# Kernel optimization log

Hardware: AMD Instinct MI355X
Metric: run time of the kernel (lower is better)

## Reference

```python
import jax, jax.numpy as jnp
import numpy as np

B, T, D_IN, H, E = 256, 512, 256, 256, 96  # batch, enc seq, input_size, hidden_size, num_embeddings


def setup_inputs() -> dict:
    key = jax.random.key(0)
    ks = jax.random.split(key, 12)
    s = 0.05
    return {
        "prev_h": jax.random.normal(ks[0], (B, H), jnp.float32),
        "prev_c": jax.random.normal(ks[1], (B, H), jnp.float32),
        "batch_H": jax.random.normal(ks[2], (B, T, D_IN), jnp.float32),
        "char_onehots": jax.random.uniform(ks[3], (B, E), jnp.float32),
        "W_i2h": jax.random.normal(ks[4], (H, D_IN), jnp.float32) * s,
        "W_h2h": jax.random.normal(ks[5], (H, H), jnp.float32) * s,
        "b_h2h": jax.random.normal(ks[6], (H,), jnp.float32) * s,
        "W_score": jax.random.normal(ks[7], (1, H), jnp.float32) * s,
        "W_ih": jax.random.normal(ks[8], (4 * H, D_IN + E), jnp.float32) * s,
        "W_hh": jax.random.normal(ks[9], (4 * H, H), jnp.float32) * s,
        "b_ih": jax.random.normal(ks[10], (4 * H,), jnp.float32) * s,
        "b_hh": jax.random.normal(ks[11], (4 * H,), jnp.float32) * s,
    }


def reference(prev_h, prev_c, batch_H, char_onehots,
              W_i2h, W_h2h, b_h2h, W_score, W_ih, W_hh, b_ih, b_hh):
    # additive attention over encoder features
    proj = jnp.einsum('btd,hd->bth', batch_H, W_i2h)          # [B,T,H]
    hid = prev_h @ W_h2h.T + b_h2h                             # [B,H]
    e = jnp.einsum('bth,oh->bto', jnp.tanh(proj + hid[:, None, :]), W_score)  # [B,T,1]
    alpha = jax.nn.softmax(e, axis=1)                          # [B,T,1]
    context = jnp.einsum('bt,btd->bd', alpha[..., 0], batch_H) # [B,D_IN]
    x = jnp.concatenate([context, char_onehots], axis=1)       # [B,D_IN+E]
    # LSTM cell step (PyTorch gate order: i, f, g, o)
    gates = x @ W_ih.T + b_ih + prev_h @ W_hh.T + b_hh         # [B,4H]
    i, f, g, o = jnp.split(gates, 4, axis=1)
    c_new = jax.nn.sigmoid(f) * prev_c + jax.nn.sigmoid(i) * jnp.tanh(g)
    h_new = jax.nn.sigmoid(o) * jnp.tanh(c_new)
    return (h_new, c_new, jnp.swapaxes(alpha, 1, 2))           # alpha -> [B,1,T]
```

## Files before the change

### kernel.cpp

```cpp
#include <hip/hip_runtime.h>

typedef __attribute__((ext_vector_type(8))) short short8;
typedef __attribute__((ext_vector_type(4))) float f32x4;

#define KPAD 40

#define WS_HID 0u
#define WS_P   262144u
#define WS_Z   786432u
#define WS_CTX 802816u
#define WS_WBF 1064960u

__device__ __forceinline__ unsigned cvtpk(float lo, float hi) {
    unsigned r;
    asm("v_cvt_pk_bf16_f32 %0, %1, %2" : "=v"(r) : "v"(lo), "v"(hi));
    return r;
}
__device__ __forceinline__ int4 pack8(float4 x0, float4 x1) {
    int4 q;
    q.x = (int)cvtpk(x0.x, x0.y);
    q.y = (int)cvtpk(x0.z, x0.w);
    q.z = (int)cvtpk(x1.x, x1.y);
    q.w = (int)cvtpk(x1.z, x1.w);
    return q;
}
__device__ __forceinline__ float tanh_fast(float x) {
    float e2 = __expf(2.f * x);
    return 1.f - 2.f * __builtin_amdgcn_rcpf(e2 + 1.f);
}
__device__ __forceinline__ float sigmoid_fast(float x) {
    return __builtin_amdgcn_rcpf(1.f + __expf(-x));
}

__global__ __launch_bounds__(256) void k_prep(
    const float* __restrict__ prev_h, const float* __restrict__ W_i2h,
    const float* __restrict__ W_h2h, const float* __restrict__ b_h2h,
    float* __restrict__ hid, int4* __restrict__ Wbf)
{
    int bid = blockIdx.x, tid = threadIdx.x;
    if (bid < 256) {
        __shared__ float ph[256];
        ph[tid] = prev_h[bid * 256 + tid];
        __syncthreads();
        float acc = b_h2h[tid];
        const float4* w = (const float4*)(W_h2h + tid * 256);
        #pragma unroll 8
        for (int k4 = 0; k4 < 64; ++k4) {
            float4 ww = w[k4];
            acc += ww.x * ph[k4*4+0] + ww.y * ph[k4*4+1] + ww.z * ph[k4*4+2] + ww.w * ph[k4*4+3];
        }
        hid[bid * 256 + tid] = acc;
    } else {
        int u = (bid - 256) * 256 + tid;
        int w = (u >> 11) & 3, cf = (u >> 9) & 3, ks = (u >> 6) & 7;
        int n = w * 64 + cf * 16 + (u & 15);
        int k0 = ks * 32 + ((u >> 4) & 3) * 8;
        float4 x0 = *(const float4*)(W_i2h + n * 256 + k0);
        float4 x1 = *(const float4*)(W_i2h + n * 256 + k0 + 4);
        Wbf[u] = pack8(x0, x1);
    }
}

__global__ __launch_bounds__(256, 2) void k_e(
    const float* __restrict__ BH, const int4* __restrict__ Wbf,
    const float* __restrict__ hid, const float* __restrict__ Wsc,
    float* __restrict__ p_out, float* __restrict__ zbuf)
{
    __shared__ short Afrag[2][8192];
    __shared__ float eps[2][128];

    const int tid = threadIdx.x;
    const int lane = tid & 63;
    const int w = tid >> 6;
    const int l15 = lane & 15, lg = lane >> 4;
    const int b = blockIdx.x;

    short8 breg[4][8];
    #pragma unroll
    for (int cf = 0; cf < 4; cf++)
        #pragma unroll
        for (int ks = 0; ks < 8; ks++) {
            const int4* ap = Wbf + (((w * 4 + cf) * 8 + ks) * 64 + lane);
            asm volatile("global_load_dwordx4 %0, %1, off"
                         : "=v"(breg[cf][ks]) : "v"(ap));
        }

    float4 la0[4], la1[4];
    auto issueA = [&](int t) {
        const float* base = BH + ((size_t)b * 512 + t * 32) * 256;
        #pragma unroll
        for (int q = 0; q < 4; q++) {
            int u = q * 256 + tid;
            int row = ((u >> 9) << 4) | (u & 15);
            int kb = ((u >> 6) & 7) * 32 + ((u >> 4) & 3) * 8;
            const float* p4 = base + row * 256 + kb;
            la0[q] = *(const float4*)p4;
            la1[q] = *(const float4*)(p4 + 4);
        }
    };
    auto writeA = [&](int buf) {
        #pragma unroll
        for (int q = 0; q < 4; q++) {
            int u = q * 256 + tid;
            *(int4*)&Afrag[buf][u * 8] = pack8(la0[q], la1[q]);
        }
    };

    issueA(0);
    asm volatile("s_waitcnt vmcnt(0)" ::: "memory");
    #pragma unroll
    for (int cf = 0; cf < 4; cf++)
        asm volatile("" : "+v"(breg[cf][0]), "+v"(breg[cf][1]), "+v"(breg[cf][2]),
                          "+v"(breg[cf][3]), "+v"(breg[cf][4]), "+v"(breg[cf][5]),
                          "+v"(breg[cf][6]), "+v"(breg[cf][7]));
    writeA(0);
    __syncthreads();

    float wsv[4], hd4[4];
    #pragma unroll
    for (int cf = 0; cf < 4; cf++) {
        int col = w * 64 + cf * 16 + l15;
        wsv[cf] = Wsc[col];
        hd4[cf] = hid[b * 256 + col];
    }

    for (int t = 0; t < 16; ++t) {
        const int cur = t & 1;
        if (t < 15) issueA(t + 1);

        f32x4 acc[2][4];
        #pragma unroll
        for (int rf = 0; rf < 2; rf++)
            #pragma unroll
            for (int cf = 0; cf < 4; cf++) acc[rf][cf] = (f32x4){0.f, 0.f, 0.f, 0.f};

        #pragma unroll
        for (int ks = 0; ks < 8; ++ks) {
            short8 af[2];
            #pragma unroll
            for (int rf = 0; rf < 2; rf++)
                af[rf] = *(const short8*)&Afrag[cur][(((rf * 8 + ks) * 64) + lane) * 8];
            #pragma unroll
            for (int rf = 0; rf < 2; rf++)
                #pragma unroll
                for (int cf = 0; cf < 4; cf++)
                    acc[rf][cf] = __builtin_amdgcn_mfma_f32_16x16x32_bf16(
                        af[rf], breg[cf][ks], acc[rf][cf], 0, 0, 0);
        }

        float esum[2][4];
        #pragma unroll
        for (int rf = 0; rf < 2; rf++)
            #pragma unroll
            for (int r = 0; r < 4; r++) esum[rf][r] = 0.f;
        #pragma unroll
        for (int cf = 0; cf < 4; cf++)
            #pragma unroll
            for (int rf = 0; rf < 2; rf++)
                #pragma unroll
                for (int r = 0; r < 4; r++)
                    esum[rf][r] += wsv[cf] * tanh_fast(acc[rf][cf][r] + hd4[cf]);
        #pragma unroll
        for (int rf = 0; rf < 2; rf++)
            #pragma unroll
            for (int r = 0; r < 4; r++) {
                float s = esum[rf][r];
                s += __shfl_xor(s, 1); s += __shfl_xor(s, 2);
                s += __shfl_xor(s, 4); s += __shfl_xor(s, 8);
                esum[rf][r] = s;
            }
        if (l15 == 0) {
            #pragma unroll
            for (int rf = 0; rf < 2; rf++)
                #pragma unroll
                for (int r = 0; r < 4; r++)
                    eps[cur][w * 32 + rf * 16 + lg * 4 + r] = esum[rf][r];
        }

        if (t < 15) writeA(cur ^ 1);
        __syncthreads();

        if (tid < 32) {
            float e = eps[cur][tid] + eps[cur][32 + tid] + eps[cur][64 + tid] + eps[cur][96 + tid];
            float p = __expf(e);
            p_out[b * 512 + t * 32 + tid] = p;
            float z = p;
            z += __shfl_xor(z, 1); z += __shfl_xor(z, 2); z += __shfl_xor(z, 4);
            z += __shfl_xor(z, 8); z += __shfl_xor(z, 16);
            if (tid == 0) zbuf[b * 16 + t] = z;
        }
    }
}

__global__ __launch_bounds__(256) void k_ctx(
    const float* __restrict__ p, const float* __restrict__ zbuf,
    const float* __restrict__ BH, float* __restrict__ alpha, float* __restrict__ ctx)
{
    __shared__ float pl[512];
    __shared__ float zsh[16];
    int b = blockIdx.x, t = threadIdx.x;
    if (t < 16) zsh[t] = zbuf[b * 16 + t];
    pl[t] = p[b * 512 + t];
    pl[256 + t] = p[b * 512 + 256 + t];
    __syncthreads();
    float Z = 0.f;
    #pragma unroll
    for (int i = 0; i < 16; ++i) Z += zsh[i];
    float inv = 1.f / Z;
    alpha[b * 512 + t] = pl[t] * inv;
    alpha[b * 512 + 256 + t] = pl[256 + t] * inv;
    const float* bh = BH + (size_t)b * 512 * 256 + t;
    float acc = 0.f;
    #pragma unroll 16
    for (int tt = 0; tt < 512; ++tt) acc += pl[tt] * bh[(size_t)tt * 256];
    ctx[b * 256 + t] = acc * inv;
}

__global__ __launch_bounds__(256) void k_gates_lstm(
    const float* __restrict__ ctx, const float* __restrict__ onehot,
    const float* __restrict__ prev_h, const float* __restrict__ W_ih,
    const float* __restrict__ W_hh, const float* __restrict__ b_ih,
    const float* __restrict__ b_hh, const float* __restrict__ prev_c,
    float* __restrict__ out)
{
    __shared__ char smem[20800];
    short* AlB = (short*)smem;
    short* BlB = (short*)smem + 5120;
    const int tid = threadIdx.x;
    const int lane = tid & 63;
    const int w = tid >> 6;
    const int l15 = lane & 15, lg = lane >> 4;
    const int rb = blockIdx.x * 64;
    const int hb = blockIdx.y;

    f32x4 acc[4];
    #pragma unroll
    for (int j = 0; j < 4; j++) acc[j] = (f32x4){0.f, 0.f, 0.f, 0.f};

    const int arow = tid >> 2, akg = tid & 3;
    const int rg = rb + arow;
    const int bn = tid >> 2, bq = tid & 3;
    const int np_ = hb * 64 + bn, hh_ = np_ >> 2, gg_ = np_ & 3;
    const float* wih_row = W_ih + (size_t)(gg_ * 256 + hh_) * 352;
    const float* whh_row = W_hh + (size_t)(gg_ * 256 + hh_) * 256;

    auto stageAB = [&](int kc, int bu) {
        int k0 = kc * 32 + akg * 8;
        const float4* pa;
        if (k0 < 256)      pa = (const float4*)(ctx    + rg * 256 + k0);
        else if (k0 < 352) pa = (const float4*)(onehot + rg * 96  + (k0 - 256));
        else               pa = (const float4*)(prev_h + rg * 256 + (k0 - 352));
        float4 x0 = pa[0], x1 = pa[1];
        *(int4*)&AlB[bu * 2560 + arow * KPAD + akg * 8] = pack8(x0, x1);
        int kb = kc * 32 + bq * 8;
        const float* pb = (kb < 352) ? (wih_row + kb) : (whh_row + (kb - 352));
        float4 y0 = *(const float4*)pb, y1 = *(const float4*)(pb + 4);
        *(int4*)&BlB[bu * 2560 + bn * KPAD + bq * 8] = pack8(y0, y1);
    };

    stageAB(0, 0);
    __syncthreads();

    for (int kc = 0; kc < 19; ++kc) {
        int cur = kc & 1;
        short8 af = *(const short8*)&AlB[cur * 2560 + (w * 16 + l15) * KPAD + lg * 8];
        short8 bfr[4];
        #pragma unroll
        for (int cf = 0; cf < 4; cf++)
            bfr[cf] = *(const short8*)&BlB[cur * 2560 + (cf * 16 + l15) * KPAD + lg * 8];
        if (kc < 18) stageAB(kc + 1, cur ^ 1);
        #pragma unroll
        for (int cf = 0; cf < 4; cf++)
            acc[cf] = __builtin_amdgcn_mfma_f32_16x16x32_bf16(af, bfr[cf], acc[cf], 0, 0, 0);
        __syncthreads();
    }

    float* Gt = (float*)smem;
    #pragma unroll
    for (int cf = 0; cf < 4; cf++) {
        int col = cf * 16 + l15;
        int np = hb * 64 + col;
        int hg = np >> 2, g = np & 3;
        float bias = b_ih[g * 256 + hg] + b_hh[g * 256 + hg];
        #pragma unroll
        for (int r = 0; r < 4; r++)
            Gt[(w * 16 + lg * 4 + r) * 65 + col] = acc[cf][r] + bias;
    }
    __syncthreads();

    #pragma unroll
    for (int it = 0; it < 4; ++it) {
        int elem = it * 256 + tid;
        int row = elem >> 4, hl = elem & 15;
        float gi = Gt[row * 65 + hl * 4 + 0];
        float gf = Gt[row * 65 + hl * 4 + 1];
        float gg = Gt[row * 65 + hl * 4 + 2];
        float go = Gt[row * 65 + hl * 4 + 3];
        int bg = rb + row, hglob = hb * 16 + hl;
        float cv = sigmoid_fast(gf) * prev_c[bg * 256 + hglob] + sigmoid_fast(gi) * tanh_fast(gg);
        out[bg * 256 + hglob] = sigmoid_fast(go) * tanh_fast(cv);
        out[65536 + bg * 256 + hglob] = cv;
    }
}

extern "C" void kernel_launch(void* const* d_in, const int* in_sizes, int n_in,
                              void* d_out, int out_size, void* d_ws, size_t ws_size,
                              hipStream_t stream) {
    (void)in_sizes; (void)n_in; (void)out_size; (void)ws_size;
    const float* prev_h  = (const float*)d_in[0];
    const float* prev_c  = (const float*)d_in[1];
    const float* batch_H = (const float*)d_in[2];
    const float* onehot  = (const float*)d_in[3];
    const float* W_i2h   = (const float*)d_in[4];
    const float* W_h2h   = (const float*)d_in[5];
    const float* b_h2h   = (const float*)d_in[6];
    const float* W_score = (const float*)d_in[7];
    const float* W_ih    = (const float*)d_in[8];
    const float* W_hh    = (const float*)d_in[9];
    const float* b_ih    = (const float*)d_in[10];
    const float* b_hh    = (const float*)d_in[11];

    char* ws = (char*)d_ws;
    float* hid   = (float*)(ws + WS_HID);
    float* p     = (float*)(ws + WS_P);
    float* zbuf  = (float*)(ws + WS_Z);
    float* ctx   = (float*)(ws + WS_CTX);
    int4*  Wbf   = (int4*)(ws + WS_WBF);

    float* out = (float*)d_out;
    float* alpha = out + 131072;

    hipLaunchKernelGGL(k_prep,       dim3(288),    dim3(256), 0, stream,
                       prev_h, W_i2h, W_h2h, b_h2h, hid, Wbf);
    hipLaunchKernelGGL(k_e,          dim3(256),    dim3(256), 0, stream,
                       batch_H, Wbf, hid, W_score, p, zbuf);
    hipLaunchKernelGGL(k_ctx,        dim3(256),    dim3(256), 0, stream,
                       p, zbuf, batch_H, alpha, ctx);
    hipLaunchKernelGGL(k_gates_lstm, dim3(4, 16),  dim3(256), 0, stream,
                       ctx, onehot, prev_h, W_ih, W_hh, b_ih, b_hh, prev_c, out);
}
```

Baseline: 80.19 us.

## Restructure attention score kernel: W in LDS, per-wave row tiles in registers

Measured after the change: 84.06 us. 1.05x slower.

```diff
diff --git a/kernel.cpp b/kernel.cpp
--- a/kernel.cpp
+++ b/kernel.cpp
@@ -30,6 +30,10 @@
 }
 __device__ __forceinline__ float sigmoid_fast(float x) {
     return __builtin_amdgcn_rcpf(1.f + __expf(-x));
+}
+__device__ __forceinline__ void gload16(const void* g, void* l) {
+    __builtin_amdgcn_global_load_lds((const __attribute__((address_space(1))) void*)g,
+                                     (__attribute__((address_space(3))) void*)l, 16, 0, 0);
 }
 
 __global__ __launch_bounds__(256) void k_prep(
@@ -52,8 +56,8 @@
         hid[bid * 256 + tid] = acc;
     } else {
         int u = (bid - 256) * 256 + tid;
-        int w = (u >> 11) & 3, cf = (u >> 9) & 3, ks = (u >> 6) & 7;
-        int n = w * 64 + cf * 16 + (u & 15);
+        int cf = u >> 9, ks = (u >> 6) & 7;
+        int n = cf * 16 + (u & 15);
         int k0 = ks * 32 + ((u >> 4) & 3) * 8;
         float4 x0 = *(const float4*)(W_i2h + n * 256 + k0);
         float4 x1 = *(const float4*)(W_i2h + n * 256 + k0 + 4);
@@ -61,134 +65,96 @@
     }
 }
 
-__global__ __launch_bounds__(256, 2) void k_e(
+__global__ __launch_bounds__(512, 2) void k_e(
     const float* __restrict__ BH, const int4* __restrict__ Wbf,
     const float* __restrict__ hid, const float* __restrict__ Wsc,
     float* __restrict__ p_out, float* __restrict__ zbuf)
 {
-    __shared__ short Afrag[2][8192];
-    __shared__ float eps[2][128];
+    __shared__ short Blds[65536];
+    __shared__ float zsh[8];
 
     const int tid = threadIdx.x;
     const int lane = tid & 63;
-    const int w = tid >> 6;
+    const int w8 = tid >> 6;
     const int l15 = lane & 15, lg = lane >> 4;
     const int b = blockIdx.x;
 
-    short8 breg[4][8];
+    float4 la[16];
+    auto issueA = [&](int tile) {
+        const float* base = BH + ((size_t)b * 512 + tile * 16 + l15) * 256 + lg * 8;
+        #pragma unroll
+        for (int ks = 0; ks < 8; ++ks) {
+            la[2 * ks]     = *(const float4*)(base + ks * 32);
+            la[2 * ks + 1] = *(const float4*)(base + ks * 32 + 4);
+        }
+    };
+    issueA(w8);
+
+    {
+        const char* g = (const char*)Wbf;
+        char* l = (char*)Blds;
+        #pragma unroll
+        for (int rnd = 0; rnd < 16; ++rnd)
+            gload16(g + rnd * 8192 + tid * 16, l + rnd * 8192 + tid * 16);
+    }
+
+    float wsv[16], hd[16];
     #pragma unroll
-    for (int cf = 0; cf < 4; cf++)
-        #pragma unroll
-        for (int ks = 0; ks < 8; ks++) {
-            const int4* ap = Wbf + (((w * 4 + cf) * 8 + ks) * 64 + lane);
-            asm volatile("global_load_dwordx4 %0, %1, off"
-                         : "=v"(breg[cf][ks]) : "v"(ap));
-        }
-
-    float4 la0[4], la1[4];
-    auto issueA = [&](int t) {
-        const float* base = BH + ((size_t)b * 512 + t * 32) * 256;
-        #pragma unroll
-        for (int q = 0; q < 4; q++) {
-            int u = q * 256 + tid;
-            int row = ((u >> 9) << 4) | (u & 15);
-            int kb = ((u >> 6) & 7) * 32 + ((u >> 4) & 3) * 8;
-            const float* p4 = base + row * 256 + kb;
-            la0[q] = *(const float4*)p4;
-            la1[q] = *(const float4*)(p4 + 4);
-        }
-    };
-    auto writeA = [&](int buf) {
-        #pragma unroll
-        for (int q = 0; q < 4; q++) {
-            int u = q * 256 + tid;
-            *(int4*)&Afrag[buf][u * 8] = pack8(la0[q], la1[q]);
-        }
-    };
-
-    issueA(0);
-    asm volatile("s_waitcnt vmcnt(0)" ::: "memory");
-    #pragma unroll
-    for (int cf = 0; cf < 4; cf++)
-        asm volatile("" : "+v"(breg[cf][0]), "+v"(breg[cf][1]), "+v"(breg[cf][2]),
-                          "+v"(breg[cf][3]), "+v"(breg[cf][4]), "+v"(breg[cf][5]),
-                          "+v"(breg[cf][6]), "+v"(breg[cf][7]));
-    writeA(0);
-    __syncthreads();
-
-    float wsv[4], hd4[4];
-    #pragma unroll
-    for (int cf = 0; cf < 4; cf++) {
-        int col = w * 64 + cf * 16 + l15;
-        wsv[cf] = Wsc[col];
-        hd4[cf] = hid[b * 256 + col];
-    }
-
-    for (int t = 0; t < 16; ++t) {
-        const int cur = t & 1;
-        if (t < 15) issueA(t + 1);
-
-        f32x4 acc[2][4];
-        #pragma unroll
-        for (int rf = 0; rf < 2; rf++)
+    for (int cf = 0; cf < 16; ++cf) {
+        wsv[cf] = Wsc[cf * 16 + l15];
+        hd[cf]  = hid[b * 256 + cf * 16 + l15];
+    }
+    __syncthreads();
+
+    float zacc = 0.f;
+    for (int ti = 0; ti < 4; ++ti) {
+        const int tile = ti * 8 + w8;
+        f32x4 acc[16];
+        #pragma unroll
+        for (int cf = 0; cf < 16; ++cf) acc[cf] = (f32x4){0.f, 0.f, 0.f, 0.f};
+
+        #pragma unroll
+        for (int ks = 0; ks < 8; ++ks) {
+            short8 af; *(int4*)&af = pack8(la[2 * ks], la[2 * ks + 1]);
             #pragma unroll
-            for (int cf = 0; cf < 4; cf++) acc[rf][cf] = (f32x4){0.f, 0.f, 0.f, 0.f};
-
-        #pragma unroll
-        for (int ks = 0; ks < 8; ++ks) {
-            short8 af[2];
+            for (int cf = 0; cf < 16; ++cf) {
+                short8 bfr = *(const short8*)&Blds[(cf * 512 + ks * 64 + lane) * 8];
+                acc[cf] = __builtin_amdgcn_mfma_f32_16x16x32_bf16(af, bfr, acc[cf], 0, 0, 0);
+            }
+        }
+        if (ti < 3) issueA(tile + 8);
+
+        float esum[4] = {0.f, 0.f, 0.f, 0.f};
+        #pragma unroll
+        for (int cf = 0; cf < 16; ++cf)
             #pragma unroll
-            for (int rf = 0; rf < 2; rf++)
-                af[rf] = *(const short8*)&Afrag[cur][(((rf * 8 + ks) * 64) + lane) * 8];
-            #pragma unroll
-            for (int rf = 0; rf < 2; rf++)
-                #pragma unroll
-                for (int cf = 0; cf < 4; cf++)
-                    acc[rf][cf] = __builtin_amdgcn_mfma_f32_16x16x32_bf16(
-                        af[rf], breg[cf][ks], acc[rf][cf], 0, 0, 0);
-        }
-
-        float esum[2][4];
-        #pragma unroll
-        for (int rf = 0; rf < 2; rf++)
-            #pragma unroll
-            for (int r = 0; r < 4; r++) esum[rf][r] = 0.f;
-        #pragma unroll
-        for (int cf = 0; cf < 4; cf++)
-            #pragma unroll
-            for (int rf = 0; rf < 2; rf++)
-                #pragma unroll
-                for (int r = 0; r < 4; r++)
-                    esum[rf][r] += wsv[cf] * tanh_fast(acc[rf][cf][r] + hd4[cf]);
-        #pragma unroll
-        for (int rf = 0; rf < 2; rf++)
-            #pragma unroll
-            for (int r = 0; r < 4; r++) {
-                float s = esum[rf][r];
-                s += __shfl_xor(s, 1); s += __shfl_xor(s, 2);
-                s += __shfl_xor(s, 4); s += __shfl_xor(s, 8);
-                esum[rf][r] = s;
-            }
+            for (int r = 0; r < 4; ++r)
+                esum[r] += wsv[cf] * tanh_fast(acc[cf][r] + hd[cf]);
+        #pragma unroll
+        for (int r = 0; r < 4; ++r) {
+            float s = esum[r];
+            s += __shfl_xor(s, 1); s += __shfl_xor(s, 2);
+            s += __shfl_xor(s, 4); s += __shfl_xor(s, 8);
+            esum[r] = s;
+        }
+        float ps = 0.f, p4r[4];
+        #pragma unroll
+        for (int r = 0; r < 4; ++r) { p4r[r] = __expf(esum[r]); ps += p4r[r]; }
         if (l15 == 0) {
             #pragma unroll
-            for (int rf = 0; rf < 2; rf++)
-                #pragma unroll
-                for (int r = 0; r < 4; r++)
-                    eps[cur][w * 32 + rf * 16 + lg * 4 + r] = esum[rf][r];
-        }
-
-        if (t < 15) writeA(cur ^ 1);
-        __syncthreads();
-
-        if (tid < 32) {
-            float e = eps[cur][tid] + eps[cur][32 + tid] + eps[cur][64 + tid] + eps[cur][96 + tid];
-            float p = __expf(e);
-            p_out[b * 512 + t * 32 + tid] = p;
-            float z = p;
-            z += __shfl_xor(z, 1); z += __shfl_xor(z, 2); z += __shfl_xor(z, 4);
-            z += __shfl_xor(z, 8); z += __shfl_xor(z, 16);
-            if (tid == 0) zbuf[b * 16 + t] = z;
-        }
+            for (int r = 0; r < 4; ++r)
+                p_out[b * 512 + tile * 16 + lg * 4 + r] = p4r[r];
+        }
+        ps += __shfl_xor(ps, 16); ps += __shfl_xor(ps, 32);
+        zacc += ps;
+    }
+    if (lane == 0) zsh[w8] = zacc;
+    __syncthreads();
+    if (tid == 0) {
+        float z = 0.f;
+        #pragma unroll
+        for (int i = 0; i < 8; ++i) z += zsh[i];
+        zbuf[b] = z;
     }
 }
 
@@ -197,16 +163,11 @@
     const float* __restrict__ BH, float* __restrict__ alpha, float* __restrict__ ctx)
 {
     __shared__ float pl[512];
-    __shared__ float zsh[16];
     int b = blockIdx.x, t = threadIdx.x;
-    if (t < 16) zsh[t] = zbuf[b * 16 + t];
     pl[t] = p[b * 512 + t];
     pl[256 + t] = p[b * 512 + 256 + t];
     __syncthreads();
-    float Z = 0.f;
-    #pragma unroll
-    for (int i = 0; i < 16; ++i) Z += zsh[i];
-    float inv = 1.f / Z;
+    float inv = 1.f / zbuf[b];
     alpha[b * 512 + t] = pl[t] * inv;
     alpha[b * 512 + 256 + t] = pl[256 + t] * inv;
     const float* bh = BH + (size_t)b * 512 * 256 + t;
@@ -332,7 +293,7 @@
 
     hipLaunchKernelGGL(k_prep,       dim3(288),    dim3(256), 0, stream,
                        prev_h, W_i2h, W_h2h, b_h2h, hid, Wbf);
-    hipLaunchKernelGGL(k_e,          dim3(256),    dim3(256), 0, stream,
+    hipLaunchKernelGGL(k_e,          dim3(256),    dim3(512), 0, stream,
                        batch_H, Wbf, hid, W_score, p, zbuf);
     hipLaunchKernelGGL(k_ctx,        dim3(256),    dim3(256), 0, stream,
                        p, zbuf, batch_H, alpha, ctx);
```
